# Kernel tuning notes

Measured on AMD Instinct MI355X. Metric: run time of the kernel, lower is better.

## Reference

```python
import jax, jax.numpy as jnp
import numpy as np

SCALE_MIN, SCALE_MAX = 0.01, 10.0
LN_EPS = 1e-5

B, KIN, H, C = 32, 6144, 512, 5


def _kaiming_uniform(k, shape):
    # torch kaiming_uniform_(a=sqrt(5)) on (out,in): bound = 1/sqrt(fan_in)
    bound = 1.0 / np.sqrt(shape[1])
    return jax.random.uniform(k, shape, minval=-bound, maxval=bound, dtype=jnp.float32)


def setup_inputs() -> dict:
    key = jax.random.key(0)
    ks = jax.random.split(key, 16)
    inp = {"x": jax.random.normal(ks[0], (B, KIN), dtype=jnp.float32)}
    dims = [(H, KIN), (H, H), (H, H)]
    for i, (o, n) in enumerate(dims):
        inp[f"w{i}"] = _kaiming_uniform(ks[1 + 3 * i], (o, n))
        inp[f"t{i}"] = jax.random.uniform(ks[2 + 3 * i], (o, n), minval=-1.0, maxval=1.0, dtype=jnp.float32)
        inp[f"s{i}"] = jax.random.uniform(ks[3 + 3 * i], (o, n), minval=-2.0, maxval=0.0, dtype=jnp.float32)
        inp[f"g{i}"] = jnp.ones((o,), jnp.float32)
        inp[f"b{i}"] = jnp.zeros((o,), jnp.float32)
    inp["cw"] = _kaiming_uniform(ks[10], (C, H))
    cbound = 1.0 / np.sqrt(H)
    inp["cb"] = jax.random.uniform(ks[11], (C,), minval=-cbound, maxval=cbound, dtype=jnp.float32)
    return inp


def _wavelet_linear(h, w, t, sr):
    # h: (B, in), params: (out, in)
    scale = SCALE_MIN + (SCALE_MAX - SCALE_MIN) * jax.nn.sigmoid(sr)
    s = (h[:, None, :] - t[None]) / (scale[None] + 1e-8)  # (B, out, in)
    psi = (1.0 - s * s) * jnp.exp(-0.5 * s * s)  # mexican hat
    return jnp.einsum('boi,oi->bo', psi, w)


def _layer_norm(h, g, b):
    m = jnp.mean(h, axis=-1, keepdims=True)
    v = jnp.mean(jnp.square(h - m), axis=-1, keepdims=True)
    return (h - m) * jax.lax.rsqrt(v + LN_EPS) * g + b


def reference(x, w0, t0, s0, g0, b0, w1, t1, s1, g1, b1, w2, t2, s2, g2, b2, cw, cb):
    h = x
    for (w, t, sr, g, b) in [(w0, t0, s0, g0, b0), (w1, t1, s1, g1, b1), (w2, t2, s2, g2, b2)]:
        h = _layer_norm(jax.nn.silu(_wavelet_linear(h, w, t, sr)), g, b)
    return h @ cw.T + cb
```

## Files before the change

kernel.cpp:

```cpp
#include <hip/hip_runtime.h>

#define LN_EPS 1e-5f
#define LOG2E 1.44269504f
#define NHALF_LOG2E (-0.72134752f)

#if __has_builtin(__builtin_amdgcn_exp2f)
#define EXP2F(x) __builtin_amdgcn_exp2f(x)
#else
#define EXP2F(x) __expf((x) * 0.69314718f)
#endif

template<int KIN>
__global__ __launch_bounds__(256)
void transpose_x(const float* __restrict__ x, float* __restrict__ xT)
{
    int idx = blockIdx.x * 256 + threadIdx.x;
    int i = idx >> 5, b = idx & 31;
    xT[idx] = x[b * KIN + i];
}

template<int KIN, int BLOCK, int S>
__global__ __launch_bounds__(BLOCK, 4)
void wav_layer(const float* __restrict__ xT, const float* __restrict__ w,
               const float* __restrict__ t, const float* __restrict__ s,
               float* __restrict__ part)
{
    constexpr int K4 = KIN / 4;
    constexpr int CHUNK = K4 / S;
    const int o   = blockIdx.x;
    const int si  = blockIdx.y;
    const int tid = threadIdx.x;

    const float4* __restrict__ w4 = (const float4*)w + (size_t)o * K4;
    const float4* __restrict__ t4 = (const float4*)t + (size_t)o * K4;
    const float4* __restrict__ s4 = (const float4*)s + (size_t)o * K4;
    const float4* __restrict__ x4 = (const float4*)xT;

    float acc[32];
#pragma unroll
    for (int b = 0; b < 32; ++b) acc[b] = 0.f;

    for (int i4 = si * CHUNK + tid; i4 < (si + 1) * CHUNK; i4 += BLOCK) {
        float4 wv = w4[i4], tv = t4[i4], sv = s4[i4];
        float wa[4] = {wv.x, wv.y, wv.z, wv.w};
        float ta[4] = {tv.x, tv.y, tv.z, tv.w};
        float sa[4] = {sv.x, sv.y, sv.z, sv.w};
        const float4* __restrict__ xr = x4 + (size_t)i4 * 32;
#pragma unroll
        for (int j = 0; j < 4; ++j) {
            float sig = __builtin_amdgcn_rcpf(1.f + EXP2F(-sa[j] * LOG2E));
            float inv = __builtin_amdgcn_rcpf(fmaf(9.99f, sig, 0.01000001f));
            float nti = -ta[j] * inv;
            float wj  = wa[j];
#pragma unroll
            for (int b4 = 0; b4 < 8; ++b4) {
                float4 xv = xr[j * 8 + b4];
                float xa[4] = {xv.x, xv.y, xv.z, xv.w};
#pragma unroll
                for (int k = 0; k < 4; ++k) {
                    float u  = fmaf(xa[k], inv, nti);
                    float u2 = u * u;
                    float e  = EXP2F(u2 * NHALF_LOG2E);
                    float pw = fmaf(-wj, u2, wj);
                    acc[b4 * 4 + k] = fmaf(pw, e, acc[b4 * 4 + k]);
                }
            }
        }
    }

    __shared__ float red[(BLOCK / 64) * 32];
    const int lane = tid & 63, wid = tid >> 6;
#pragma unroll
    for (int b = 0; b < 32; ++b) {
        float v = acc[b];
#pragma unroll
        for (int off = 32; off; off >>= 1) v += __shfl_down(v, off);
        if (lane == 0) red[wid * 32 + b] = v;
    }
    __syncthreads();
    if (tid < 32) {
        float v = 0.f;
#pragma unroll
        for (int k = 0; k < BLOCK / 64; ++k) v += red[k * 32 + tid];
        part[(size_t)si * 16384 + tid * 512 + o] = v;
    }
}

template<int S>
__global__ __launch_bounds__(512)
void silu_ln(const float* __restrict__ part, const float* __restrict__ g,
             const float* __restrict__ bias, float* __restrict__ hT)
{
    const int b = blockIdx.x, tid = threadIdx.x;
    float v = 0.f;
#pragma unroll
    for (int si = 0; si < S; ++si) v += part[(size_t)si * 16384 + b * 512 + tid];
    float a = v * __builtin_amdgcn_rcpf(1.f + EXP2F(-v * LOG2E));

    float s1 = a, s2 = a * a;
#pragma unroll
    for (int off = 32; off; off >>= 1) {
        s1 += __shfl_down(s1, off);
        s2 += __shfl_down(s2, off);
    }
    __shared__ float r1[8], r2[8];
    const int lane = tid & 63, wid = tid >> 6;
    if (lane == 0) { r1[wid] = s1; r2[wid] = s2; }
    __syncthreads();
    float t1 = 0.f, t2 = 0.f;
#pragma unroll
    for (int k = 0; k < 8; ++k) { t1 += r1[k]; t2 += r2[k]; }
    float m   = t1 * (1.f / 512.f);
    float var = t2 * (1.f / 512.f) - m * m;
    float r   = __builtin_amdgcn_rsqf(var + LN_EPS);
    hT[tid * 32 + b] = (a - m) * r * g[tid] + bias[tid];
}

template<int S>
__global__ __launch_bounds__(512)
void silu_ln_cls(const float* __restrict__ part, const float* __restrict__ g,
                 const float* __restrict__ bias, const float* __restrict__ cw,
                 const float* __restrict__ cb, float* __restrict__ out)
{
    const int b = blockIdx.x, tid = threadIdx.x;
    float v = 0.f;
#pragma unroll
    for (int si = 0; si < S; ++si) v += part[(size_t)si * 16384 + b * 512 + tid];
    float a = v * __builtin_amdgcn_rcpf(1.f + EXP2F(-v * LOG2E));

    float s1 = a, s2 = a * a;
#pragma unroll
    for (int off = 32; off; off >>= 1) {
        s1 += __shfl_down(s1, off);
        s2 += __shfl_down(s2, off);
    }
    __shared__ float r1[8], r2[8];
    const int lane = tid & 63, wid = tid >> 6;
    if (lane == 0) { r1[wid] = s1; r2[wid] = s2; }
    __syncthreads();
    float t1 = 0.f, t2 = 0.f;
#pragma unroll
    for (int k = 0; k < 8; ++k) { t1 += r1[k]; t2 += r2[k]; }
    float m   = t1 * (1.f / 512.f);
    float var = t2 * (1.f / 512.f) - m * m;
    float r   = __builtin_amdgcn_rsqf(var + LN_EPS);
    float hl  = (a - m) * r * g[tid] + bias[tid];

    __shared__ float cr[5][8];
#pragma unroll
    for (int c = 0; c < 5; ++c) {
        float pv = hl * cw[c * 512 + tid];
#pragma unroll
        for (int off = 32; off; off >>= 1) pv += __shfl_down(pv, off);
        if (lane == 0) cr[c][wid] = pv;
    }
    __syncthreads();
    if (tid < 5) {
        float sum = 0.f;
#pragma unroll
        for (int k = 0; k < 8; ++k) sum += cr[tid][k];
        out[b * 5 + tid] = sum + cb[tid];
    }
}

extern "C" void kernel_launch(void* const* d_in, const int* in_sizes, int n_in,
                              void* d_out, int out_size, void* d_ws, size_t ws_size,
                              hipStream_t stream)
{
    const float* x  = (const float*)d_in[0];
    const float* w0 = (const float*)d_in[1];
    const float* t0 = (const float*)d_in[2];
    const float* s0 = (const float*)d_in[3];
    const float* g0 = (const float*)d_in[4];
    const float* b0 = (const float*)d_in[5];
    const float* w1 = (const float*)d_in[6];
    const float* t1 = (const float*)d_in[7];
    const float* s1 = (const float*)d_in[8];
    const float* g1 = (const float*)d_in[9];
    const float* b1 = (const float*)d_in[10];
    const float* w2 = (const float*)d_in[11];
    const float* t2 = (const float*)d_in[12];
    const float* s2 = (const float*)d_in[13];
    const float* g2 = (const float*)d_in[14];
    const float* b2 = (const float*)d_in[15];
    const float* cw = (const float*)d_in[16];
    const float* cb = (const float*)d_in[17];
    float* out = (float*)d_out;

    float* xT   = (float*)d_ws;
    float* part = xT + 196608;
    float* hT   = part + 6 * 16384;

    transpose_x<6144><<<768, 256, 0, stream>>>(x, xT);
    wav_layer<6144, 256, 6><<<dim3(512, 6), 256, 0, stream>>>(xT, w0, t0, s0, part);
    silu_ln<6><<<32, 512, 0, stream>>>(part, g0, b0, hT);
    wav_layer<512, 128, 1><<<dim3(512, 1), 128, 0, stream>>>(hT, w1, t1, s1, part);
    silu_ln<1><<<32, 512, 0, stream>>>(part, g1, b1, hT);
    wav_layer<512, 128, 1><<<dim3(512, 1), 128, 0, stream>>>(hT, w2, t2, s2, part);
    silu_ln_cls<1><<<32, 512, 0, stream>>>(part, g2, b2, cw, cb, out);
}
```

Measured before the change: 204.0 us.

## Restructure wavelet layer: per-wave output rows, shared-memory precomputed params, finer K split

Each 64-lane wave now handles one output row. The per-input sigmoid and reciprocal scale terms are precomputed once into shared memory, instead of being recomputed inside the batch loop. Each lane accumulates only two batch elements, replacing the 32-accumulator-per-thread scheme and its 32 cross-wave reductions. The K dimension is split 16 ways for layer 0 and 8 ways for the small layers to raise occupancy. The partial-sum layout is changed to [split][o][b], which increases partial-sum traffic and the number of terms summed in the LayerNorm kernels.

```diff
diff --git a/kernel.cpp b/kernel.cpp
--- a/kernel.cpp
+++ b/kernel.cpp
@@ -19,70 +19,61 @@
     xT[idx] = x[b * KIN + i];
 }
 
-template<int KIN, int BLOCK, int S>
-__global__ __launch_bounds__(BLOCK, 4)
+template<int KIN, int S>
+__global__ __launch_bounds__(128, 6)
 void wav_layer(const float* __restrict__ xT, const float* __restrict__ w,
                const float* __restrict__ t, const float* __restrict__ s,
                float* __restrict__ part)
 {
-    constexpr int K4 = KIN / 4;
-    constexpr int CHUNK = K4 / S;
-    const int o   = blockIdx.x;
-    const int si  = blockIdx.y;
-    const int tid = threadIdx.x;
+    constexpr int RANGE = KIN / S;
+    constexpr int STEPS = RANGE / 4;
+    constexpr int PREPS = RANGE / 64;
+    __shared__ float4 prep[2][RANGE];
 
-    const float4* __restrict__ w4 = (const float4*)w + (size_t)o * K4;
-    const float4* __restrict__ t4 = (const float4*)t + (size_t)o * K4;
-    const float4* __restrict__ s4 = (const float4*)s + (size_t)o * K4;
-    const float4* __restrict__ x4 = (const float4*)xT;
+    const int wave = threadIdx.x >> 6;
+    const int lane = threadIdx.x & 63;
+    const int o    = (blockIdx.x << 1) + wave;
+    const int si   = blockIdx.y;
+    const int ibase = si * RANGE;
 
-    float acc[32];
+    const float* __restrict__ wp = w + (size_t)o * KIN + ibase;
+    const float* __restrict__ tp = t + (size_t)o * KIN + ibase;
+    const float* __restrict__ sp = s + (size_t)o * KIN + ibase;
+
 #pragma unroll
-    for (int b = 0; b < 32; ++b) acc[b] = 0.f;
+    for (int r = 0; r < PREPS; ++r) {
+        int il = r * 64 + lane;
+        float wv = wp[il], tv = tp[il], sv = sp[il];
+        float sig = __builtin_amdgcn_rcpf(1.f + EXP2F(-sv * LOG2E));
+        float inv = __builtin_amdgcn_rcpf(fmaf(9.99f, sig, 0.01000001f));
+        prep[wave][il] = make_float4(inv, -tv * inv, wv, 0.f);
+    }
+    __syncthreads();
 
-    for (int i4 = si * CHUNK + tid; i4 < (si + 1) * CHUNK; i4 += BLOCK) {
-        float4 wv = w4[i4], tv = t4[i4], sv = s4[i4];
-        float wa[4] = {wv.x, wv.y, wv.z, wv.w};
-        float ta[4] = {tv.x, tv.y, tv.z, tv.w};
-        float sa[4] = {sv.x, sv.y, sv.z, sv.w};
-        const float4* __restrict__ xr = x4 + (size_t)i4 * 32;
-#pragma unroll
-        for (int j = 0; j < 4; ++j) {
-            float sig = __builtin_amdgcn_rcpf(1.f + EXP2F(-sa[j] * LOG2E));
-            float inv = __builtin_amdgcn_rcpf(fmaf(9.99f, sig, 0.01000001f));
-            float nti = -ta[j] * inv;
-            float wj  = wa[j];
-#pragma unroll
-            for (int b4 = 0; b4 < 8; ++b4) {
-                float4 xv = xr[j * 8 + b4];
-                float xa[4] = {xv.x, xv.y, xv.z, xv.w};
-#pragma unroll
-                for (int k = 0; k < 4; ++k) {
-                    float u  = fmaf(xa[k], inv, nti);
-                    float u2 = u * u;
-                    float e  = EXP2F(u2 * NHALF_LOG2E);
-                    float pw = fmaf(-wj, u2, wj);
-                    acc[b4 * 4 + k] = fmaf(pw, e, acc[b4 * 4 + k]);
-                }
-            }
-        }
+    const int p = lane & 15, g = lane >> 4;
+    const float2* __restrict__ xp = (const float2*)xT + (size_t)(ibase + g) * 16 + p;
+
+    float acc0 = 0.f, acc1 = 0.f;
+#pragma unroll 4
+    for (int st = 0; st < STEPS; ++st) {
+        float4 pr = prep[wave][st * 4 + g];
+        float2 xv = xp[(size_t)st * 64];
+        float u0 = fmaf(xv.x, pr.x, pr.y);
+        float u1 = fmaf(xv.y, pr.x, pr.y);
+        float q0 = u0 * u0, q1 = u1 * u1;
+        float e0 = EXP2F(q0 * NHALF_LOG2E);
+        float e1 = EXP2F(q1 * NHALF_LOG2E);
+        float pw0 = fmaf(-pr.z, q0, pr.z);
+        float pw1 = fmaf(-pr.z, q1, pr.z);
+        acc0 = fmaf(pw0, e0, acc0);
+        acc1 = fmaf(pw1, e1, acc1);
     }
 
-    __shared__ float red[(BLOCK / 64) * 32];
-    const int lane = tid & 63, wid = tid >> 6;
-#pragma unroll
-    for (int b = 0; b < 32; ++b) {
-        float v = acc[b];
-#pragma unroll
-        for (int off = 32; off; off >>= 1) v += __shfl_down(v, off);
-        if (lane == 0) red[wid * 32 + b] = v;
-    }
-    __syncthreads();
-    if (tid < 32) {
-        float v = 0.f;
-#pragma unroll
-        for (int k = 0; k < BLOCK / 64; ++k) v += red[k * 32 + tid];
-        part[(size_t)si * 16384 + tid * 512 + o] = v;
+    acc0 += __shfl_down(acc0, 32); acc0 += __shfl_down(acc0, 16);
+    acc1 += __shfl_down(acc1, 32); acc1 += __shfl_down(acc1, 16);
+    if (lane < 16) {
+        float2* pp = (float2*)(part + (size_t)si * 16384 + o * 32) + p;
+        *pp = make_float2(acc0, acc1);
     }
 }
 
@@ -94,7 +85,7 @@
     const int b = blockIdx.x, tid = threadIdx.x;
     float v = 0.f;
 #pragma unroll
-    for (int si = 0; si < S; ++si) v += part[(size_t)si * 16384 + b * 512 + tid];
+    for (int si = 0; si < S; ++si) v += part[(size_t)si * 16384 + tid * 32 + b];
     float a = v * __builtin_amdgcn_rcpf(1.f + EXP2F(-v * LOG2E));
 
     float s1 = a, s2 = a * a;
@@ -125,7 +116,7 @@
     const int b = blockIdx.x, tid = threadIdx.x;
     float v = 0.f;
 #pragma unroll
-    for (int si = 0; si < S; ++si) v += part[(size_t)si * 16384 + b * 512 + tid];
+    for (int si = 0; si < S; ++si) v += part[(size_t)si * 16384 + tid * 32 + b];
     float a = v * __builtin_amdgcn_rcpf(1.f + EXP2F(-v * LOG2E));
 
     float s1 = a, s2 = a * a;
@@ -189,13 +180,13 @@
 
     float* xT   = (float*)d_ws;
     float* part = xT + 196608;
-    float* hT   = part + 6 * 16384;
+    float* hT   = part + 16 * 16384;
 
     transpose_x<6144><<<768, 256, 0, stream>>>(x, xT);
-    wav_layer<6144, 256, 6><<<dim3(512, 6), 256, 0, stream>>>(xT, w0, t0, s0, part);
-    silu_ln<6><<<32, 512, 0, stream>>>(part, g0, b0, hT);
-    wav_layer<512, 128, 1><<<dim3(512, 1), 128, 0, stream>>>(hT, w1, t1, s1, part);
-    silu_ln<1><<<32, 512, 0, stream>>>(part, g1, b1, hT);
-    wav_layer<512, 128, 1><<<dim3(512, 1), 128, 0, stream>>>(hT, w2, t2, s2, part);
-    silu_ln_cls<1><<<32, 512, 0, stream>>>(part, g2, b2, cw, cb, out);
+    wav_layer<6144, 16><<<dim3(256, 16), 128, 0, stream>>>(xT, w0, t0, s0, part);
+    silu_ln<16><<<32, 512, 0, stream>>>(part, g0, b0, hT);
+    wav_layer<512, 8><<<dim3(256, 8), 128, 0, stream>>>(hT, w1, t1, s1, part);
+    silu_ln<8><<<32, 512, 0, stream>>>(part, g1, b1, hT);
+    wav_layer<512, 8><<<dim3(256, 8), 128, 0, stream>>>(hT, w2, t2, s2, part);
+    silu_ln_cls<8><<<32, 512, 0, stream>>>(part, g2, b2, cw, cb, out);
 }
```

After: 175.1 us. -14.2%, faster.
